# Performance work log

Measured on AMD Instinct MI355X. Metric: run time of the kernel, lower is better.

## Reference

```python
import jax, jax.numpy as jnp
import numpy as np

B, S, D, H = 2, 2048, 1024, 16
DH = D // H
NEG = -1000000000.0


def setup_inputs() -> dict:
    key = jax.random.key(0)
    ks = jax.random.split(key, 8)
    q = jax.random.normal(ks[0], (B, S, D), dtype=jnp.float32)
    k = jax.random.normal(ks[1], (B, S, D), dtype=jnp.float32)
    v = jax.random.normal(ks[2], (B, S, D), dtype=jnp.float32)
    # padding mask [B, k_len]; ensure first key position is valid
    mask = jax.random.randint(ks[3], (B, S), 0, 2, dtype=jnp.int32)
    mask = mask.at[:, 0].set(1)
    scale = 1.0 / np.sqrt(D)
    Wq = jax.random.normal(ks[4], (D, D), dtype=jnp.float32) * scale
    Wk = jax.random.normal(ks[5], (D, D), dtype=jnp.float32) * scale
    Wv = jax.random.normal(ks[6], (D, D), dtype=jnp.float32) * scale
    Wo = jax.random.normal(ks[7], (D, D), dtype=jnp.float32) * scale
    return {"q": q, "k": k, "v": v, "mask": mask,
            "Wq": Wq, "Wk": Wk, "Wv": Wv, "Wo": Wo}


def reference(q, k, v, mask, Wq, Wk, Wv, Wo):
    # nn.Linear(bias=False): y = x @ W.T  (W is [out, in])
    Q = jnp.einsum('bsd,ed->bse', q, Wq)
    K = jnp.einsum('bsd,ed->bse', k, Wk)
    V = jnp.einsum('bsd,ed->bse', v, Wv)
    # split heads -> [B, H, S, DH]
    Q = Q.reshape(B, S, H, DH).transpose(0, 2, 1, 3)
    K = K.reshape(B, S, H, DH).transpose(0, 2, 1, 3)
    V = V.reshape(B, S, H, DH).transpose(0, 2, 1, 3)
    scores = jnp.einsum('bhqd,bhkd->bhqk', Q, K) / jnp.float32(np.sqrt(DH))
    # padding mask: [B, K] -> additive [B, 1, 1, K]
    pad = jnp.where(mask == 0, jnp.float32(NEG), jnp.float32(0.0))[:, None, None, :]
    scores = scores + pad
    # causal (mask_future=True): strict upper triangle blocked
    causal = jnp.where(jnp.triu(jnp.ones((S, S), dtype=bool), k=1),
                       jnp.float32(NEG), jnp.float32(0.0))
    scores = scores + causal
    attn = jax.nn.softmax(scores, axis=-1)
    out = jnp.einsum('bhqk,bhkd->bhqd', attn, V)  # [B, H, S, DH]
    out = out.transpose(0, 2, 1, 3).reshape(B, S, D)
    out = jnp.einsum('bsd,ed->bse', out, Wo)
    # dropout: identity in eval mode
    return out
```

## Files before the change

kernel.cpp:

```cpp
#include <hip/hip_runtime.h>
#include <stdint.h>

#define BB 2
#define SS 2048
#define DD 1024
#define HH 16
#define DHH 64

typedef __bf16 bf16_t;
typedef bf16_t bf16x8 __attribute__((ext_vector_type(8)));
typedef float f32x4 __attribute__((ext_vector_type(4)));

union FragU { uint4 u; bf16x8 b; };

__device__ __forceinline__ unsigned short f2bf(float f) {
  union { float f; unsigned int u; } x; x.f = f;
  unsigned int u = x.u;
  return (unsigned short)((u + 0x7FFFu + ((u >> 16) & 1u)) >> 16);
}

__device__ __forceinline__ uint2 pack4(float4 v) {
  uint2 r;
  r.x = (unsigned)f2bf(v.x) | ((unsigned)f2bf(v.y) << 16);
  r.y = (unsigned)f2bf(v.z) | ((unsigned)f2bf(v.w) << 16);
  return r;
}

__device__ __forceinline__ bf16x8 ldsFrag(const unsigned short* s, int idx) {
  FragU f;
  f.u = *reinterpret_cast<const uint4*>(s + idx);
  return f.b;
}

__device__ __forceinline__ void gload_lds16(const unsigned short* g, unsigned short* s) {
  __builtin_amdgcn_global_load_lds(
      (const __attribute__((address_space(1))) unsigned int*)g,
      (__attribute__((address_space(3))) unsigned int*)s, 16, 0, 0);
}

#define MFMA16(a, b, c) __builtin_amdgcn_mfma_f32_16x16x32_bf16((a), (b), (c), 0, 0, 0)

__global__ __launch_bounds__(256) void convert_kernel(
    const float* __restrict__ q, const float* __restrict__ k, const float* __restrict__ v,
    const float* __restrict__ Wq, const float* __restrict__ Wk,
    const float* __restrict__ Wv, const float* __restrict__ Wo,
    unsigned short* __restrict__ Ab, unsigned short* __restrict__ Wb) {
  const int z = blockIdx.y;
  const float* src;
  unsigned short* dst;
  float scale = 1.0f;
  if (z < 3) {
    src = (z == 0) ? q : (z == 1) ? k : v;
    dst = Ab + (size_t)z * BB * SS * DD;
  } else {
    if (blockIdx.x >= (DD * DD / 1024)) return;
    src = (z == 3) ? Wq : (z == 4) ? Wk : (z == 5) ? Wv : Wo;
    dst = Wb + (size_t)(z - 3) * DD * DD;
    if (z == 3) scale = 0.125f;
  }
  const size_t base = (size_t)blockIdx.x * 1024 + (size_t)threadIdx.x * 4;
  float4 val = *reinterpret_cast<const float4*>(src + base);
  val.x *= scale; val.y *= scale; val.z *= scale; val.w *= scale;
  uint2 p = pack4(val);
  *reinterpret_cast<uint2*>(dst + base) = p;
}

__global__ __launch_bounds__(256) void proj128_kernel(
    const unsigned short* __restrict__ Ab, const unsigned short* __restrict__ Wb,
    unsigned short* __restrict__ Qb, unsigned short* __restrict__ Kb,
    unsigned short* __restrict__ Vt) {
  __shared__ unsigned short sA[128 * 64];
  __shared__ unsigned short sB[128 * 64];

  const int z = blockIdx.z;
  const unsigned short* A = Ab + (size_t)z * BB * SS * DD;
  const unsigned short* W = Wb + (size_t)z * DD * DD;
  unsigned short* Out = (z == 0) ? Qb : (z == 1) ? Kb : Vt;
  const int layout = (z == 2) ? 1 : 0;

  const int t = threadIdx.x;
  const int lane = t & 63, wave = t >> 6;
  const int quad = lane >> 4, l15 = lane & 15;
  const int wr = wave >> 1, wc = wave & 1;
  const int mBase = blockIdx.x * 128, nBase = blockIdx.y * 128;

  f32x4 acc[4][4] = {};

  for (int k0 = 0; k0 < DD; k0 += 64) {
    #pragma unroll
    for (int i = 0; i < 4; ++i) {
      const int g = wave * 4 + i;
      const int row = g * 8 + (lane >> 3);
      const int oct = (lane & 7) ^ (row & 7);
      gload_lds16(A + (size_t)(mBase + row) * DD + k0 + oct * 8, &sA[g * 512]);
      gload_lds16(W + (size_t)(nBase + row) * DD + k0 + oct * 8, &sB[g * 512]);
    }
    __syncthreads();

    #pragma unroll
    for (int kk = 0; kk < 2; ++kk) {
      bf16x8 af[4], bfr[4];
      #pragma unroll
      for (int i = 0; i < 4; ++i) {
        const int row = wr * 64 + i * 16 + l15;
        af[i] = ldsFrag(sA, (row * 8 + ((kk * 4 + quad) ^ (l15 & 7))) * 8);
      }
      #pragma unroll
      for (int j = 0; j < 4; ++j) {
        const int row = wc * 64 + j * 16 + l15;
        bfr[j] = ldsFrag(sB, (row * 8 + ((kk * 4 + quad) ^ (l15 & 7))) * 8);
      }
      #pragma unroll
      for (int i = 0; i < 4; ++i)
        #pragma unroll
        for (int j = 0; j < 4; ++j)
          acc[i][j] = MFMA16(af[i], bfr[j], acc[i][j]);
    }
    __syncthreads();
  }

  #pragma unroll
  for (int i = 0; i < 4; ++i) {
    #pragma unroll
    for (int j = 0; j < 4; ++j) {
      #pragma unroll
      for (int r = 0; r < 4; ++r) {
        int m = mBase + wr * 64 + i * 16 + quad * 4 + r;
        int n = nBase + wc * 64 + j * 16 + l15;
        int b = m >> 11, s = m & (SS - 1);
        int h = n >> 6, dh = n & (DHH - 1);
        size_t off;
        if (layout == 0)
          off = ((size_t)(b * HH + h) * SS + s) * DHH + dh;
        else
          off = ((size_t)(b * HH + h) * DHH + dh) * SS + s;
        Out[off] = f2bf(acc[i][j][r]);
      }
    }
  }
}

__global__ __launch_bounds__(256) void attn_kernel(
    const unsigned short* __restrict__ Qb, const unsigned short* __restrict__ Kb,
    const unsigned short* __restrict__ Vt, const int* __restrict__ mask,
    unsigned short* __restrict__ Ob) {
  __shared__ __align__(16) char smem[16384 + 16384 + 17408];
  unsigned short* sK  = (unsigned short*)smem;
  unsigned short* sV  = (unsigned short*)(smem + 16384);
  unsigned short* sPT = (unsigned short*)(smem + 32768);
  unsigned short* sQ  = sPT;

  const int t = threadIdx.x;
  const int lane = t & 63, wave = t >> 6;
  const int quad = lane >> 4, l15 = lane & 15;
  const int h = blockIdx.y, b = blockIdx.z;
  const size_t headOff = (size_t)(b * HH + h) * SS * DHH;
  const unsigned short* Qh = Qb + headOff;
  const unsigned short* Kh = Kb + headOff;
  const unsigned short* Vh = Vt + headOff;
  const int* maskp = mask + b * SS;

  FragU onesU;
  onesU.u.x = 0x3F803F80u; onesU.u.y = 0x3F803F80u;
  onesU.u.z = 0x3F803F80u; onesU.u.w = 0x3F803F80u;
  const bf16x8 ones = onesU.b;

  #pragma unroll
  for (int phase = 0; phase < 2; ++phase) {
    const int qt = (phase == 0) ? (int)blockIdx.x : (int)(31 - blockIdx.x);
    const int qb = qt * 64;

    #pragma unroll
    for (int i = 0; i < 2; ++i) {
      const int g = wave * 2 + i;
      const int row = g * 8 + (lane >> 3);
      const int oct = (lane & 7) ^ (row & 7);
      gload_lds16(Qh + (size_t)(qb + row) * DHH + oct * 8, &sQ[g * 512]);
    }
    __syncthreads();

    bf16x8 aq[2];
    #pragma unroll
    for (int kk = 0; kk < 2; ++kk) {
      const int row = wave * 16 + l15;
      aq[kk] = ldsFrag(sQ, (row * 8 + ((kk * 4 + quad) ^ (l15 & 7))) * 8);
    }

    float m_r[4];
    f32x4 oacc[5] = {};
    #pragma unroll
    for (int r = 0; r < 4; ++r) m_r[r] = -1e30f;

    const int nc = (qt + 2) >> 1;
    const int qrow0 = qb + wave * 16 + quad * 4;
    for (int c = 0; c < nc; ++c) {
      const int c0 = c * 128;
      #pragma unroll
      for (int i = 0; i < 4; ++i) {
        const int g = wave * 4 + i;
        const int row = g * 8 + (lane >> 3);
        const int oct = (lane & 7) ^ (row & 7);
        gload_lds16(Kh + (size_t)(c0 + row) * DHH + oct * 8, &sK[g * 512]);
      }
      #pragma unroll
      for (int i = 0; i < 4; ++i) {
        const int g = wave * 4 + i;
        const int row = g * 4 + (lane >> 4);
        const int oct = (lane & 15) ^ (row & 15);
        gload_lds16(Vh + (size_t)row * SS + c0 + oct * 8, &sV[g * 512]);
      }
      float padmul[8];
      #pragma unroll
      for (int j = 0; j < 8; ++j)
        padmul[j] = (float)maskp[c0 + j * 16 + l15];
      __syncthreads();

      f32x4 sacc[8] = {};
      #pragma unroll
      for (int kk = 0; kk < 2; ++kk) {
        #pragma unroll
        for (int j = 0; j < 8; ++j) {
          const int row = j * 16 + l15;
          bf16x8 bk = ldsFrag(sK, (row * 8 + ((kk * 4 + quad) ^ (l15 & 7))) * 8);
          sacc[j] = MFMA16(aq[kk], bk, sacc[j]);
        }
      }

      float mnew[4], alpha[4];
      #pragma unroll
      for (int r = 0; r < 4; ++r) {
        float rm = fmaxf(fmaxf(fmaxf(sacc[0][r], sacc[1][r]), fmaxf(sacc[2][r], sacc[3][r])),
                         fmaxf(fmaxf(sacc[4][r], sacc[5][r]), fmaxf(sacc[6][r], sacc[7][r])));
        #pragma unroll
        for (int off = 1; off < 16; off <<= 1)
          rm = fmaxf(rm, __shfl_xor(rm, off));
        mnew[r] = fmaxf(m_r[r], rm);
        alpha[r] = __expf(m_r[r] - mnew[r]);
        m_r[r] = mnew[r];
      }

      const bool diag = (c == nc - 1);
      #pragma unroll
      for (int j = 0; j < 8; ++j) {
        float p0 = __expf(sacc[j][0] - mnew[0]) * padmul[j];
        float p1 = __expf(sacc[j][1] - mnew[1]) * padmul[j];
        float p2 = __expf(sacc[j][2] - mnew[2]) * padmul[j];
        float p3 = __expf(sacc[j][3] - mnew[3]) * padmul[j];
        if (diag) {
          const int kcol = c0 + j * 16 + l15;
          p0 = (kcol > qrow0 + 0) ? 0.0f : p0;
          p1 = (kcol > qrow0 + 1) ? 0.0f : p1;
          p2 = (kcol > qrow0 + 2) ? 0.0f : p2;
          p3 = (kcol > qrow0 + 3) ? 0.0f : p3;
        }
        uint2 w;
        w.x = __builtin_amdgcn_perm(__float_as_uint(p1), __float_as_uint(p0), 0x07060302u);
        w.y = __builtin_amdgcn_perm(__float_as_uint(p3), __float_as_uint(p2), 0x07060302u);
        *reinterpret_cast<uint2*>(&sPT[(j * 16 + l15) * 68 + wave * 16 + quad * 4]) = w;
      }

      #pragma unroll
      for (int jn = 0; jn < 5; ++jn)
        #pragma unroll
        for (int r = 0; r < 4; ++r)
          oacc[jn][r] *= alpha[r];

      #pragma unroll
      for (int kk = 0; kk < 4; ++kk) {
        bf16x8 ap;
        #pragma unroll
        for (int jj = 0; jj < 8; ++jj)
          ap[jj] = *reinterpret_cast<const bf16_t*>(
              &sPT[(kk * 32 + quad * 8 + jj) * 68 + wave * 16 + l15]);
        #pragma unroll
        for (int jn = 0; jn < 4; ++jn) {
          const int row = jn * 16 + l15;
          bf16x8 bv = ldsFrag(sV, (row * 16 + ((kk * 4 + quad) ^ l15)) * 8);
          oacc[jn] = MFMA16(ap, bv, oacc[jn]);
        }
        oacc[4] = MFMA16(ap, ones, oacc[4]);
      }
      __syncthreads();
    }

    #pragma unroll
    for (int r = 0; r < 4; ++r) {
      const float inv = 1.0f / oacc[4][r];
      const int qrow = qrow0 + r;
      #pragma unroll
      for (int jn = 0; jn < 4; ++jn) {
        const int col = h * DHH + jn * 16 + l15;
        Ob[(size_t)(b * SS + qrow) * DD + col] = f2bf(oacc[jn][r] * inv);
      }
    }
  }
}

__global__ __launch_bounds__(256) void outproj_kernel(
    const unsigned short* __restrict__ Ag, const unsigned short* __restrict__ Wb,
    float* __restrict__ Out) {
  __shared__ unsigned short sA[128 * 64];
  __shared__ unsigned short sB[128 * 64];

  const unsigned short* W = Wb + (size_t)3 * DD * DD;
  const int t = threadIdx.x;
  const int lane = t & 63, wave = t >> 6;
  const int quad = lane >> 4, l15 = lane & 15;
  const int wr = wave >> 1, wc = wave & 1;
  const int mBase = blockIdx.x * 128, nBase = blockIdx.y * 128;

  f32x4 acc[4][4] = {};

  for (int k0 = 0; k0 < DD; k0 += 64) {
    #pragma unroll
    for (int i = 0; i < 4; ++i) {
      const int g = wave * 4 + i;
      const int row = g * 8 + (lane >> 3);
      const int oct = (lane & 7) ^ (row & 7);
      gload_lds16(Ag + (size_t)(mBase + row) * DD + k0 + oct * 8, &sA[g * 512]);
      gload_lds16(W + (size_t)(nBase + row) * DD + k0 + oct * 8, &sB[g * 512]);
    }
    __syncthreads();

    #pragma unroll
    for (int kk = 0; kk < 2; ++kk) {
      bf16x8 af[4], bfr[4];
      #pragma unroll
      for (int i = 0; i < 4; ++i) {
        const int row = wr * 64 + i * 16 + l15;
        af[i] = ldsFrag(sA, (row * 8 + ((kk * 4 + quad) ^ (l15 & 7))) * 8);
      }
      #pragma unroll
      for (int j = 0; j < 4; ++j) {
        const int row = wc * 64 + j * 16 + l15;
        bfr[j] = ldsFrag(sB, (row * 8 + ((kk * 4 + quad) ^ (l15 & 7))) * 8);
      }
      #pragma unroll
      for (int i = 0; i < 4; ++i)
        #pragma unroll
        for (int j = 0; j < 4; ++j)
          acc[i][j] = MFMA16(af[i], bfr[j], acc[i][j]);
    }
    __syncthreads();
  }

  #pragma unroll
  for (int i = 0; i < 4; ++i) {
    #pragma unroll
    for (int j = 0; j < 4; ++j) {
      #pragma unroll
      for (int r = 0; r < 4; ++r) {
        int m = mBase + wr * 64 + i * 16 + quad * 4 + r;
        int n = nBase + wc * 64 + j * 16 + l15;
        Out[(size_t)m * DD + n] = acc[i][j][r];
      }
    }
  }
}

extern "C" void kernel_launch(void* const* d_in, const int* in_sizes, int n_in,
                              void* d_out, int out_size, void* d_ws, size_t ws_size,
                              hipStream_t stream) {
  (void)in_sizes; (void)n_in; (void)out_size; (void)ws_size;
  const float* q  = (const float*)d_in[0];
  const float* k  = (const float*)d_in[1];
  const float* v  = (const float*)d_in[2];
  const int* mask = (const int*)d_in[3];
  const float* Wq = (const float*)d_in[4];
  const float* Wk = (const float*)d_in[5];
  const float* Wv = (const float*)d_in[6];
  const float* Wo = (const float*)d_in[7];
  float* out = (float*)d_out;

  const size_t AE = (size_t)BB * SS * DD;
  unsigned short* Ab = (unsigned short*)d_ws;
  unsigned short* Ob = Ab;
  unsigned short* Wb = Ab + 3 * AE;
  unsigned short* Qb = Wb + (size_t)4 * DD * DD;
  unsigned short* Kb = Qb + AE;
  unsigned short* Vt = Kb + AE;

  convert_kernel<<<dim3(AE / 1024, 7), 256, 0, stream>>>(q, k, v, Wq, Wk, Wv, Wo, Ab, Wb);

  proj128_kernel<<<dim3(BB * SS / 128, DD / 128, 3), 256, 0, stream>>>(
      Ab, Wb, Qb, Kb, Vt);

  attn_kernel<<<dim3(SS / 128, HH, BB), 256, 0, stream>>>(Qb, Kb, Vt, mask, Ob);

  outproj_kernel<<<dim3(BB * SS / 128, DD / 128), 256, 0, stream>>>(Ob, Wb, out);
}
```

Measured before the change: 237.6 us.

## Restructure attention to transposed S, register-resident P, exp2 softmax and XCD-aware grid

Attention now computes S transposed (K as the A operand), so each lane owns one query row. The bf16 P tile stays in registers and feeds a 16x16x16 MFMA directly, which removes the LDS round-trip for P and the ones-MFMA used for the row sum. Softmax uses exp2 with log2e folded into the Wq scale and adds a precomputed additive float pad mask built in the convert kernel. The grid is flattened to one 64-row query tile per block and remapped so each XCD covers whole heads with heavy tiles first; launch bounds allow 4 blocks per CU. Output is staged through LDS for coalesced 16-byte stores, at the cost of the old two-phase load balancing within a block.

After: 254.3 us. 7.0% more time.

```diff
diff --git a/kernel.cpp b/kernel.cpp
--- a/kernel.cpp
+++ b/kernel.cpp
@@ -10,8 +10,16 @@
 typedef __bf16 bf16_t;
 typedef bf16_t bf16x8 __attribute__((ext_vector_type(8)));
 typedef float f32x4 __attribute__((ext_vector_type(4)));
+typedef short s16x4 __attribute__((ext_vector_type(4)));
 
 union FragU { uint4 u; bf16x8 b; };
+union Frag4U { uint2 u; s16x4 s; };
+
+#if __has_builtin(__builtin_amdgcn_exp2f)
+#define EXP2(x) __builtin_amdgcn_exp2f(x)
+#else
+#define EXP2(x) exp2f(x)
+#endif
 
 __device__ __forceinline__ unsigned short f2bf(float f) {
   union { float f; unsigned int u; } x; x.f = f;
@@ -39,13 +47,28 @@
 }
 
 #define MFMA16(a, b, c) __builtin_amdgcn_mfma_f32_16x16x32_bf16((a), (b), (c), 0, 0, 0)
+#define MFMA16K16(a, b, c) __builtin_amdgcn_mfma_f32_16x16x16bf16_1k((a), (b), (c), 0, 0, 0)
 
 __global__ __launch_bounds__(256) void convert_kernel(
     const float* __restrict__ q, const float* __restrict__ k, const float* __restrict__ v,
     const float* __restrict__ Wq, const float* __restrict__ Wk,
     const float* __restrict__ Wv, const float* __restrict__ Wo,
-    unsigned short* __restrict__ Ab, unsigned short* __restrict__ Wb) {
+    const int* __restrict__ mask,
+    unsigned short* __restrict__ Ab, unsigned short* __restrict__ Wb,
+    float* __restrict__ Mf) {
   const int z = blockIdx.y;
+  if (z == 7) {
+    if (blockIdx.x >= 4) return;
+    const size_t base = (size_t)blockIdx.x * 1024 + (size_t)threadIdx.x * 4;
+    int4 m4 = *reinterpret_cast<const int4*>(mask + base);
+    float4 p;
+    p.x = (m4.x == 0) ? -1.0e9f : 0.0f;
+    p.y = (m4.y == 0) ? -1.0e9f : 0.0f;
+    p.z = (m4.z == 0) ? -1.0e9f : 0.0f;
+    p.w = (m4.w == 0) ? -1.0e9f : 0.0f;
+    *reinterpret_cast<float4*>(Mf + base) = p;
+    return;
+  }
   const float* src;
   unsigned short* dst;
   float scale = 1.0f;
@@ -56,7 +79,7 @@
     if (blockIdx.x >= (DD * DD / 1024)) return;
     src = (z == 3) ? Wq : (z == 4) ? Wk : (z == 5) ? Wv : Wo;
     dst = Wb + (size_t)(z - 3) * DD * DD;
-    if (z == 3) scale = 0.125f;
+    if (z == 3) scale = 0.125f * 1.44269504088896f;
   }
   const size_t base = (size_t)blockIdx.x * 1024 + (size_t)threadIdx.x * 4;
   float4 val = *reinterpret_cast<const float4*>(src + base);
@@ -140,159 +163,148 @@
   }
 }
 
-__global__ __launch_bounds__(256) void attn_kernel(
+__global__ __launch_bounds__(256, 4) void attn_kernel(
     const unsigned short* __restrict__ Qb, const unsigned short* __restrict__ Kb,
-    const unsigned short* __restrict__ Vt, const int* __restrict__ mask,
+    const unsigned short* __restrict__ Vt, const float* __restrict__ Mf,
     unsigned short* __restrict__ Ob) {
-  __shared__ __align__(16) char smem[16384 + 16384 + 17408];
-  unsigned short* sK  = (unsigned short*)smem;
-  unsigned short* sV  = (unsigned short*)(smem + 16384);
-  unsigned short* sPT = (unsigned short*)(smem + 32768);
-  unsigned short* sQ  = sPT;
+  __shared__ __align__(16) char smem[32768];
+  unsigned short* sK = (unsigned short*)smem;
+  unsigned short* sV = (unsigned short*)(smem + 16384);
+  unsigned short* sO = (unsigned short*)smem;
 
   const int t = threadIdx.x;
   const int lane = t & 63, wave = t >> 6;
   const int quad = lane >> 4, l15 = lane & 15;
-  const int h = blockIdx.y, b = blockIdx.z;
-  const size_t headOff = (size_t)(b * HH + h) * SS * DHH;
+
+  const int id = blockIdx.x;
+  const int xcd = id & 7, rest = id >> 3;
+  const int hd = xcd * 4 + (rest >> 5);
+  const int qt = 31 - (rest & 31);
+  const int b = hd >> 4, h = hd & 15;
+  const int qb = qt * 64;
+
+  const size_t headOff = (size_t)hd * SS * DHH;
   const unsigned short* Qh = Qb + headOff;
   const unsigned short* Kh = Kb + headOff;
   const unsigned short* Vh = Vt + headOff;
-  const int* maskp = mask + b * SS;
-
-  FragU onesU;
-  onesU.u.x = 0x3F803F80u; onesU.u.y = 0x3F803F80u;
-  onesU.u.z = 0x3F803F80u; onesU.u.w = 0x3F803F80u;
-  const bf16x8 ones = onesU.b;
-
-  #pragma unroll
-  for (int phase = 0; phase < 2; ++phase) {
-    const int qt = (phase == 0) ? (int)blockIdx.x : (int)(31 - blockIdx.x);
-    const int qb = qt * 64;
-
-    #pragma unroll
-    for (int i = 0; i < 2; ++i) {
-      const int g = wave * 2 + i;
+  const float* Mp = Mf + b * SS;
+
+  bf16x8 aq[2];
+  {
+    const unsigned short* qp = Qh + (size_t)(qb + wave * 16 + l15) * DHH + quad * 8;
+    FragU f0, f1;
+    f0.u = *reinterpret_cast<const uint4*>(qp);
+    f1.u = *reinterpret_cast<const uint4*>(qp + 32);
+    aq[0] = f0.b; aq[1] = f1.b;
+  }
+
+  float m_l = -1.0e30f, l_l = 0.0f;
+  f32x4 oacc[4] = {};
+  const int nc = (qt + 2) >> 1;
+  const int qrow_abs = qb + wave * 16 + l15;
+
+  for (int c = 0; c < nc; ++c) {
+    const int c0 = c * 128;
+    #pragma unroll
+    for (int i = 0; i < 4; ++i) {
+      const int g = wave * 4 + i;
       const int row = g * 8 + (lane >> 3);
       const int oct = (lane & 7) ^ (row & 7);
-      gload_lds16(Qh + (size_t)(qb + row) * DHH + oct * 8, &sQ[g * 512]);
-    }
-    __syncthreads();
-
-    bf16x8 aq[2];
+      gload_lds16(Kh + (size_t)(c0 + row) * DHH + oct * 8, &sK[g * 512]);
+    }
+    #pragma unroll
+    for (int i = 0; i < 4; ++i) {
+      const int g = wave * 4 + i;
+      const int row = g * 4 + (lane >> 4);
+      const int oct = (lane & 15) ^ (row & 15);
+      gload_lds16(Vh + (size_t)row * SS + c0 + oct * 8, &sV[g * 512]);
+    }
+    __syncthreads();
+
+    f32x4 sacc[8] = {};
     #pragma unroll
     for (int kk = 0; kk < 2; ++kk) {
-      const int row = wave * 16 + l15;
-      aq[kk] = ldsFrag(sQ, (row * 8 + ((kk * 4 + quad) ^ (l15 & 7))) * 8);
-    }
-
-    float m_r[4];
-    f32x4 oacc[5] = {};
-    #pragma unroll
-    for (int r = 0; r < 4; ++r) m_r[r] = -1e30f;
-
-    const int nc = (qt + 2) >> 1;
-    const int qrow0 = qb + wave * 16 + quad * 4;
-    for (int c = 0; c < nc; ++c) {
-      const int c0 = c * 128;
-      #pragma unroll
-      for (int i = 0; i < 4; ++i) {
-        const int g = wave * 4 + i;
-        const int row = g * 8 + (lane >> 3);
-        const int oct = (lane & 7) ^ (row & 7);
-        gload_lds16(Kh + (size_t)(c0 + row) * DHH + oct * 8, &sK[g * 512]);
-      }
-      #pragma unroll
-      for (int i = 0; i < 4; ++i) {
-        const int g = wave * 4 + i;
-        const int row = g * 4 + (lane >> 4);
-        const int oct = (lane & 15) ^ (row & 15);
-        gload_lds16(Vh + (size_t)row * SS + c0 + oct * 8, &sV[g * 512]);
-      }
-      float padmul[8];
-      #pragma unroll
-      for (int j = 0; j < 8; ++j)
-        padmul[j] = (float)maskp[c0 + j * 16 + l15];
-      __syncthreads();
-
-      f32x4 sacc[8] = {};
-      #pragma unroll
-      for (int kk = 0; kk < 2; ++kk) {
-        #pragma unroll
-        for (int j = 0; j < 8; ++j) {
-          const int row = j * 16 + l15;
-          bf16x8 bk = ldsFrag(sK, (row * 8 + ((kk * 4 + quad) ^ (l15 & 7))) * 8);
-          sacc[j] = MFMA16(aq[kk], bk, sacc[j]);
-        }
-      }
-
-      float mnew[4], alpha[4];
-      #pragma unroll
-      for (int r = 0; r < 4; ++r) {
-        float rm = fmaxf(fmaxf(fmaxf(sacc[0][r], sacc[1][r]), fmaxf(sacc[2][r], sacc[3][r])),
-                         fmaxf(fmaxf(sacc[4][r], sacc[5][r]), fmaxf(sacc[6][r], sacc[7][r])));
-        #pragma unroll
-        for (int off = 1; off < 16; off <<= 1)
-          rm = fmaxf(rm, __shfl_xor(rm, off));
-        mnew[r] = fmaxf(m_r[r], rm);
-        alpha[r] = __expf(m_r[r] - mnew[r]);
-        m_r[r] = mnew[r];
-      }
-
-      const bool diag = (c == nc - 1);
       #pragma unroll
       for (int j = 0; j < 8; ++j) {
-        float p0 = __expf(sacc[j][0] - mnew[0]) * padmul[j];
-        float p1 = __expf(sacc[j][1] - mnew[1]) * padmul[j];
-        float p2 = __expf(sacc[j][2] - mnew[2]) * padmul[j];
-        float p3 = __expf(sacc[j][3] - mnew[3]) * padmul[j];
-        if (diag) {
-          const int kcol = c0 + j * 16 + l15;
-          p0 = (kcol > qrow0 + 0) ? 0.0f : p0;
-          p1 = (kcol > qrow0 + 1) ? 0.0f : p1;
-          p2 = (kcol > qrow0 + 2) ? 0.0f : p2;
-          p3 = (kcol > qrow0 + 3) ? 0.0f : p3;
-        }
-        uint2 w;
-        w.x = __builtin_amdgcn_perm(__float_as_uint(p1), __float_as_uint(p0), 0x07060302u);
-        w.y = __builtin_amdgcn_perm(__float_as_uint(p3), __float_as_uint(p2), 0x07060302u);
-        *reinterpret_cast<uint2*>(&sPT[(j * 16 + l15) * 68 + wave * 16 + quad * 4]) = w;
-      }
-
-      #pragma unroll
-      for (int jn = 0; jn < 5; ++jn)
-        #pragma unroll
-        for (int r = 0; r < 4; ++r)
-          oacc[jn][r] *= alpha[r];
-
-      #pragma unroll
-      for (int kk = 0; kk < 4; ++kk) {
-        bf16x8 ap;
-        #pragma unroll
-        for (int jj = 0; jj < 8; ++jj)
-          ap[jj] = *reinterpret_cast<const bf16_t*>(
-              &sPT[(kk * 32 + quad * 8 + jj) * 68 + wave * 16 + l15]);
-        #pragma unroll
-        for (int jn = 0; jn < 4; ++jn) {
-          const int row = jn * 16 + l15;
-          bf16x8 bv = ldsFrag(sV, (row * 16 + ((kk * 4 + quad) ^ l15)) * 8);
-          oacc[jn] = MFMA16(ap, bv, oacc[jn]);
-        }
-        oacc[4] = MFMA16(ap, ones, oacc[4]);
-      }
-      __syncthreads();
-    }
-
-    #pragma unroll
-    for (int r = 0; r < 4; ++r) {
-      const float inv = 1.0f / oacc[4][r];
-      const int qrow = qrow0 + r;
+        const int row = j * 16 + l15;
+        bf16x8 ak = ldsFrag(sK, (row * 8 + ((kk * 4 + quad) ^ (l15 & 7))) * 8);
+        sacc[j] = MFMA16(ak, aq[kk], sacc[j]);
+      }
+    }
+
+    float rm = -1.0e30f;
+    #pragma unroll
+    for (int j = 0; j < 8; ++j)
+      rm = fmaxf(rm, fmaxf(fmaxf(sacc[j][0], sacc[j][1]), fmaxf(sacc[j][2], sacc[j][3])));
+    rm = fmaxf(rm, __shfl_xor(rm, 16));
+    rm = fmaxf(rm, __shfl_xor(rm, 32));
+    const float mnew = fmaxf(m_l, rm);
+    const float alpha = EXP2(m_l - mnew);
+    m_l = mnew;
+
+    const bool diag = (c == nc - 1);
+    float rs = 0.0f;
+    s16x4 pk[8];
+    #pragma unroll
+    for (int j = 0; j < 8; ++j) {
+      float4 pf = *reinterpret_cast<const float4*>(Mp + c0 + j * 16 + quad * 4);
+      float p0 = EXP2(sacc[j][0] - mnew + pf.x);
+      float p1 = EXP2(sacc[j][1] - mnew + pf.y);
+      float p2 = EXP2(sacc[j][2] - mnew + pf.z);
+      float p3 = EXP2(sacc[j][3] - mnew + pf.w);
+      if (diag) {
+        const int key = c0 + j * 16 + quad * 4;
+        p0 = (key + 0 > qrow_abs) ? 0.0f : p0;
+        p1 = (key + 1 > qrow_abs) ? 0.0f : p1;
+        p2 = (key + 2 > qrow_abs) ? 0.0f : p2;
+        p3 = (key + 3 > qrow_abs) ? 0.0f : p3;
+      }
+      rs += (p0 + p1) + (p2 + p3);
+      Frag4U fu;
+      fu.u.x = __builtin_amdgcn_perm(__float_as_uint(p1) + 0x8000u,
+                                     __float_as_uint(p0) + 0x8000u, 0x07060302u);
+      fu.u.y = __builtin_amdgcn_perm(__float_as_uint(p3) + 0x8000u,
+                                     __float_as_uint(p2) + 0x8000u, 0x07060302u);
+      pk[j] = fu.s;
+    }
+    rs += __shfl_xor(rs, 16);
+    rs += __shfl_xor(rs, 32);
+    l_l = l_l * alpha + rs;
+
+    #pragma unroll
+    for (int jn = 0; jn < 4; ++jn)
+      oacc[jn] *= alpha;
+
+    #pragma unroll
+    for (int j = 0; j < 8; ++j) {
       #pragma unroll
       for (int jn = 0; jn < 4; ++jn) {
-        const int col = h * DHH + jn * 16 + l15;
-        Ob[(size_t)(b * SS + qrow) * DD + col] = f2bf(oacc[jn][r] * inv);
-      }
-    }
+        const int row = jn * 16 + l15;
+        const int unit = row * 16 + ((2 * j + (quad >> 1)) ^ l15);
+        Frag4U av;
+        av.u = *reinterpret_cast<const uint2*>(&sV[unit * 8 + (quad & 1) * 4]);
+        oacc[jn] = MFMA16K16(av.s, pk[j], oacc[jn]);
+      }
+    }
+    __syncthreads();
+  }
+
+  const float inv = 1.0f / l_l;
+  #pragma unroll
+  for (int jn = 0; jn < 4; ++jn) {
+    uint2 w;
+    w.x = (unsigned)f2bf(oacc[jn][0] * inv) | ((unsigned)f2bf(oacc[jn][1] * inv) << 16);
+    w.y = (unsigned)f2bf(oacc[jn][2] * inv) | ((unsigned)f2bf(oacc[jn][3] * inv) << 16);
+    *reinterpret_cast<uint2*>(&sO[(wave * 16 + l15) * 72 + jn * 16 + quad * 4]) = w;
+  }
+  __syncthreads();
+  {
+    const int row = t >> 2, seg = t & 3;
+    uint4 u0 = *reinterpret_cast<const uint4*>(&sO[row * 72 + seg * 16]);
+    uint4 u1 = *reinterpret_cast<const uint4*>(&sO[row * 72 + seg * 16 + 8]);
+    unsigned short* dst = Ob + (size_t)(b * SS + qb + row) * DD + h * DHH + seg * 16;
+    *reinterpret_cast<uint4*>(dst) = u0;
+    *reinterpret_cast<uint4*>(dst + 8) = u1;
   }
 }
 
@@ -379,13 +391,15 @@
   unsigned short* Qb = Wb + (size_t)4 * DD * DD;
   unsigned short* Kb = Qb + AE;
   unsigned short* Vt = Kb + AE;
-
-  convert_kernel<<<dim3(AE / 1024, 7), 256, 0, stream>>>(q, k, v, Wq, Wk, Wv, Wo, Ab, Wb);
+  float* Mf = (float*)(Vt + AE);
+
+  convert_kernel<<<dim3(AE / 1024, 8), 256, 0, stream>>>(
+      q, k, v, Wq, Wk, Wv, Wo, mask, Ab, Wb, Mf);
 
   proj128_kernel<<<dim3(BB * SS / 128, DD / 128, 3), 256, 0, stream>>>(
       Ab, Wb, Qb, Kb, Vt);
 
-  attn_kernel<<<dim3(SS / 128, HH, BB), 256, 0, stream>>>(Qb, Kb, Vt, mask, Ob);
+  attn_kernel<<<dim3(32 * HH * BB), 256, 0, stream>>>(Qb, Kb, Vt, Mf, Ob);
 
   outproj_kernel<<<dim3(BB * SS / 128, DD / 128), 256, 0, stream>>>(Ob, Wb, out);
 }
```
